# Optimization experiments

Measured on AMD Instinct MI355X. Metric: run time of the kernel, lower is better.

## Reference

```python
import jax, jax.numpy as jnp
import numpy as np

V, E, U, L = 32000, 512, 1024, 2  # vocab, embed_dim, units, layers
B, T = 64, 256


def setup_inputs() -> dict:
    key = jax.random.key(0)
    ks = jax.random.split(key, 8)
    s = lambda k, shape: jax.random.normal(k, shape, jnp.float32) * 0.02
    return {
        "tokens": jax.random.randint(ks[0], (B, T), 0, V),
        "emb": s(ks[1], (V, E)),
        "W0": s(ks[2], (E, 4 * U)), "U0": s(ks[3], (U, 4 * U)),
        "b0": jnp.zeros((4 * U,), jnp.float32),
        "W1": s(ks[4], (U, 4 * U)), "U1": s(ks[5], (U, 4 * U)),
        "b1": jnp.zeros((4 * U,), jnp.float32),
    }


def _lstm_layer(x, W, Uw, b):
    # x: [B,T,D]. Precompute all input projections: [T,B,4U] (batched GEMM outside scan).
    xz = jnp.einsum('btd,dg->tbg', x, W) + b
    units = Uw.shape[0]

    def step(carry, xz_t):
        h, c = carry
        z = xz_t + h @ Uw  # [B,4U]
        i, f, g, o = jnp.split(z, 4, axis=-1)  # Keras gate order: i,f,c,o
        i = jax.nn.sigmoid(i)
        f = jax.nn.sigmoid(f)
        g = jnp.tanh(g)
        o = jax.nn.sigmoid(o)
        c = f * c + i * g
        h = o * jnp.tanh(c)
        return (h, c), h

    h0 = jnp.zeros((x.shape[0], units), x.dtype)
    (h, c), ys = jax.lax.scan(step, (h0, h0), xz)
    return jnp.transpose(ys, (1, 0, 2)), h, c  # [B,T,U], [B,U], [B,U]


def reference(tokens, emb, W0, U0, b0, W1, U1, b1):
    x = emb[tokens]  # [B,T,E] embedding lookup
    x, h, c = _lstm_layer(x, W0, U0, b0)
    x, h, c = _lstm_layer(x, W1, U1, b1)
    # Keras: return_sequences=True, return_state=True -> (seq, h_last, c_last) of last layer
    return (x, h, c)
```

## Files before the change

### kernel.cpp

```cpp
#include <hip/hip_runtime.h>


typedef _Float16 f16;
typedef _Float16 f16x8 __attribute__((ext_vector_type(8)));
typedef _Float16 f16x4 __attribute__((ext_vector_type(4)));
typedef float f32x4 __attribute__((ext_vector_type(4)));

__device__ __forceinline__ f32x4 mfma16x32(f16x8 a, f16x8 b, f32x4 c) {
  return __builtin_amdgcn_mfma_f32_16x16x32_f16(a, b, c, 0, 0, 0);
}

__device__ __forceinline__ void gl_lds16(const void* g, void* l) {
  __builtin_amdgcn_global_load_lds(
      (const __attribute__((address_space(1))) void*)g,
      (__attribute__((address_space(3))) void*)l, 16, 0, 0);
}

__device__ __forceinline__ float sigmoidf_(float x) {
  return 1.0f / (1.0f + expf(-x));
}

__device__ __forceinline__ void st_f16_sc(f16* p, float v) {
  f16 h = (f16)v;
  unsigned u = (unsigned)__builtin_bit_cast(unsigned short, h);
  asm volatile("global_store_short %0, %1, off sc0 sc1"
               :: "v"(p), "v"(u) : "memory");
}
__device__ __forceinline__ void st_b128_sc(f16* p, f16x8 v) {
  asm volatile("global_store_dwordx4 %0, %1, off sc0 sc1"
               :: "v"(p), "v"(v) : "memory");
}

__device__ __forceinline__ unsigned ld_flag(const unsigned* p) {
  return __hip_atomic_load(p, __ATOMIC_RELAXED, __HIP_MEMORY_SCOPE_AGENT);
}
__device__ __forceinline__ void st_flag(unsigned* p, unsigned v) {
  __hip_atomic_store(p, v, __ATOMIC_RELAXED, __HIP_MEMORY_SCOPE_AGENT);
}

__global__ __launch_bounds__(256) void k_transpose_f16(
    const float* __restrict__ S, f16* __restrict__ D, int K, int N) {
  __shared__ float tile[64][65];
  int nk = K >> 6;
  int k0 = (blockIdx.x % nk) << 6;
  int n0 = (blockIdx.x / nk) << 6;
  int tc = threadIdx.x & 63;
  int tq = threadIdx.x >> 6;
#pragma unroll
  for (int r = 0; r < 16; ++r) {
    int kk = tq * 16 + r;
    tile[kk][tc] = S[(size_t)(k0 + kk) * N + (n0 + tc)];
  }
  __syncthreads();
#pragma unroll
  for (int r = 0; r < 16; ++r) {
    int nn = tq * 16 + r;
    D[(size_t)(n0 + nn) * K + (k0 + tc)] = (f16)tile[tc][nn];
  }
}

__global__ __launch_bounds__(256) void k_embed_f16(
    const int* __restrict__ tok, const float* __restrict__ emb,
    f16* __restrict__ A0) {
  int i = blockIdx.x * 256 + threadIdx.x;
  int m = i >> 7;
  int e = (i & 127) << 2;
  int t = m >> 6, b = m & 63;
  int tk = tok[b * 256 + t];
  const float4 v = *(const float4*)(emb + (size_t)tk * 512 + e);
  f16x4 o = {(f16)v.x, (f16)v.y, (f16)v.z, (f16)v.w};
  *(f16x4*)(A0 + (size_t)m * 512 + e) = o;
}

__global__ __launch_bounds__(256) void k_gemm_f16(
    const f16* __restrict__ A, const f16* __restrict__ Bt,
    const float* __restrict__ bias, f16* __restrict__ C,
    int M, int N, int K) {
  __shared__ f16 sA[2][128 * 32];
  __shared__ f16 sB[2][128 * 32];
  const int tid = threadIdx.x, lane = tid & 63, w = tid >> 6;
  const int mb = M >> 7;
  const int bm = blockIdx.x % mb, bn = blockIdx.x / mb;
  const int am0 = bm << 7, bn0 = bn << 7;
  const int wm = w >> 1, wn = w & 1;
  const int srow = lane >> 2, sch = lane & 3;

  f32x4 acc[4][4] = {};
  const int NT = K >> 5;
  int cur = 0;

  auto stage = [&](int kt, int buf) {
#pragma unroll
    for (int q2 = 0; q2 < 2; ++q2) {
      int q = w * 2 + q2;
      int row = q * 16 + srow;
      const f16* ga = A + (size_t)(am0 + row) * K + kt * 32 + sch * 8;
      const f16* gb = Bt + (size_t)(bn0 + row) * K + kt * 32 + sch * 8;
      gl_lds16(ga, (char*)&sA[buf][0] + q * 1024);
      gl_lds16(gb, (char*)&sB[buf][0] + q * 1024);
    }
  };

  stage(0, 0);
  __syncthreads();
  for (int kt = 0; kt < NT; ++kt) {
    if (kt + 1 < NT) stage(kt + 1, cur ^ 1);
    const f16* pa = &sA[cur][(wm * 64 + (lane & 15)) * 32 + (lane >> 4) * 8];
    const f16* pb = &sB[cur][(wn * 64 + (lane & 15)) * 32 + (lane >> 4) * 8];
    f16x8 av[4], bv[4];
#pragma unroll
    for (int mf = 0; mf < 4; ++mf) av[mf] = *(const f16x8*)(pa + mf * 512);
#pragma unroll
    for (int nf = 0; nf < 4; ++nf) bv[nf] = *(const f16x8*)(pb + nf * 512);
#pragma unroll
    for (int mf = 0; mf < 4; ++mf)
#pragma unroll
      for (int nf = 0; nf < 4; ++nf)
        acc[mf][nf] = mfma16x32(av[mf], bv[nf], acc[mf][nf]);
    __syncthreads();
    cur ^= 1;
  }

#pragma unroll
  for (int mf = 0; mf < 4; ++mf)
#pragma unroll
    for (int nf = 0; nf < 4; ++nf) {
      int col = bn0 + wn * 64 + nf * 16 + (lane & 15);
      float bs = bias[col];
#pragma unroll
      for (int r = 0; r < 4; ++r) {
        int row = am0 + wm * 64 + mf * 16 + (lane >> 4) * 4 + r;
        C[(size_t)row * N + col] = (f16)(acc[mf][nf][r] + bs);
      }
    }
}

__global__ __launch_bounds__(256, 2) void k_scan8(
    const f16* __restrict__ XZ, const f16* __restrict__ U0t,
    const f16* __restrict__ W1t, const f16* __restrict__ U1t,
    const float* __restrict__ b1, f16* __restrict__ A1,
    f16* __restrict__ H1h, float* __restrict__ out, unsigned* arr) {
  __shared__ float zred[4224];
  __shared__ __align__(16) f16 hstage[16][16];
  const int tid = threadIdx.x, lane = tid & 63, w = tid >> 6;
  const int j = lane & 15, kg = lane >> 4;
  const int l = (int)blockIdx.x >> 8;
  const int rb = (int)blockIdx.x & 255;
  const int q = rb >> 6, i = rb & 63;
  const int cc = ((i & 7) << 3) + (i >> 3);
  const int u0 = cc * 16, row0 = q * 16;
  const int wko = w * 256 + kg * 8;
  const int aoff = (row0 + j) * 1024 + wko;
  const int erl = tid >> 4, eunit = tid & 15;
  const int erow = row0 + erl, eu = u0 + eunit;
  unsigned* gArr = arr + (size_t)((l * 4 + q) * 64) * 32;
  unsigned* l0Arr = arr + (size_t)(q * 64) * 32;

  f16x8 bv[4][8];
  {
    const f16* RW = l ? U1t : U0t;
#pragma unroll
    for (int n = 0; n < 4; ++n) {
      const f16* bp = RW + (size_t)(n * 1024 + u0 + j) * 1024 + wko;
#pragma unroll
      for (int kt = 0; kt < 8; ++kt)
        bv[n][kt] = *(const f16x8*)(bp + kt * 32);
    }
  }
  float c = 0.0f;

  if (l == 0) {
    float xz[4];
#pragma unroll
    for (int g = 0; g < 4; ++g)
      xz[g] = (float)XZ[(size_t)erow * 4096 + g * 1024 + eu];

    for (int s = 0; s < 256; ++s) {
      f32x4 acc[4] = {};
      if (s > 0) {
        const f16* ap = A1 + (size_t)(s - 1) * 65536 + aoff;
#pragma unroll
        for (int kt = 0; kt < 8; ++kt) {
          f16x8 av = *(const f16x8*)(ap + kt * 32);
#pragma unroll
          for (int n = 0; n < 4; ++n)
            acc[n] = mfma16x32(av, bv[n][kt], acc[n]);
        }
      }
#pragma unroll
      for (int n = 0; n < 4; ++n)
#pragma unroll
        for (int r = 0; r < 4; ++r)
          zred[w * 1056 + (kg * 4 + r) * 66 + n * 16 + j] = acc[n][r];
      __syncthreads();
      float z[4];
#pragma unroll
      for (int g = 0; g < 4; ++g) {
        float sm = xz[g];
#pragma unroll
        for (int wv = 0; wv < 4; ++wv)
          sm += zred[wv * 1056 + erl * 66 + g * 16 + eunit];
        z[g] = sm;
      }
      float gi = sigmoidf_(z[0]), gf = sigmoidf_(z[1]);
      float gg = tanhf(z[2]), go = sigmoidf_(z[3]);
      c = gf * c + gi * gg;
      hstage[erl][eunit] = (f16)(go * tanhf(c));
      __syncthreads();
      if (tid < 32)
        st_b128_sc(&A1[(size_t)(s * 64 + row0 + (tid >> 1)) * 1024 + u0 +
                       (tid & 1) * 8],
                   *(const f16x8*)&hstage[tid >> 1][(tid & 1) * 8]);
      asm volatile("s_waitcnt vmcnt(0)" ::: "memory");
      __syncthreads();

      const unsigned v = (unsigned)s + 1u;
      if (tid == 0) st_flag(&gArr[(unsigned)i * 32u], v);
      float xzn[4] = {0.f, 0.f, 0.f, 0.f};
      if (s + 1 < 256) {
        const f16* xrow = XZ + (size_t)((s + 1) * 64 + erow) * 4096;
#pragma unroll
        for (int g = 0; g < 4; ++g) xzn[g] = (float)xrow[g * 1024 + eu];
      }
      if (tid < 64) {
        while (ld_flag(&gArr[(unsigned)tid * 32u]) < v)
          __builtin_amdgcn_s_sleep(1);
      }
      __syncthreads();
#pragma unroll
      for (int g = 0; g < 4; ++g) xz[g] = xzn[g];
    }
  } else {
    float bias1[4];
#pragma unroll
    for (int g = 0; g < 4; ++g) bias1[g] = b1[g * 1024 + eu];
    const f16* w1p[4];
#pragma unroll
    for (int n = 0; n < 4; ++n)
      w1p[n] = W1t + (size_t)(n * 1024 + u0 + j) * 1024 + wko;

    if (tid < 64) {
      while (ld_flag(&l0Arr[(unsigned)tid * 32u]) < 1u)
        __builtin_amdgcn_s_sleep(1);
    }
    __syncthreads();
    f32x4 accW[4] = {};
    {
      const f16* ap = A1 + aoff;
#pragma unroll
      for (int kt = 0; kt < 8; ++kt) {
        f16x8 av = *(const f16x8*)(ap + kt * 32);
#pragma unroll
        for (int n = 0; n < 4; ++n)
          accW[n] = mfma16x32(av, *(const f16x8*)(w1p[n] + kt * 32),
                              accW[n]);
      }
    }

    for (int t = 0; t < 256; ++t) {
      f32x4 acc[4] = {accW[0], accW[1], accW[2], accW[3]};
      if (t > 0) {
        const f16* hp = H1h + (size_t)(t - 1) * 65536 + aoff;
#pragma unroll
        for (int kt = 0; kt < 8; ++kt) {
          f16x8 av = *(const f16x8*)(hp + kt * 32);
#pragma unroll
          for (int n = 0; n < 4; ++n)
            acc[n] = mfma16x32(av, bv[n][kt], acc[n]);
        }
      }
#pragma unroll
      for (int n = 0; n < 4; ++n)
#pragma unroll
        for (int r = 0; r < 4; ++r)
          zred[w * 1056 + (kg * 4 + r) * 66 + n * 16 + j] = acc[n][r];
      __syncthreads();
      float z[4];
#pragma unroll
      for (int g = 0; g < 4; ++g) {
        float sm = bias1[g];
#pragma unroll
        for (int wv = 0; wv < 4; ++wv)
          sm += zred[wv * 1056 + erl * 66 + g * 16 + eunit];
        z[g] = sm;
      }
      float gi = sigmoidf_(z[0]), gf = sigmoidf_(z[1]);
      float gg = tanhf(z[2]), go = sigmoidf_(z[3]);
      c = gf * c + gi * gg;
      float hn = go * tanhf(c);
      if (t == 255) {
        out[(size_t)erow * 262144 + (size_t)t * 1024 + eu] = hn;
        out[16777216 + erow * 1024 + eu] = hn;
        out[16777216 + 65536 + erow * 1024 + eu] = c;
        break;
      }
      hstage[erl][eunit] = (f16)hn;
      __syncthreads();
      if (tid < 32)
        st_b128_sc(&H1h[(size_t)t * 65536 + (row0 + (tid >> 1)) * 1024 + u0 +
                        (tid & 1) * 8],
                   *(const f16x8*)&hstage[tid >> 1][(tid & 1) * 8]);
      asm volatile("s_waitcnt vmcnt(0)" ::: "memory");
      __syncthreads();

      const unsigned v = (unsigned)t + 1u;
      if (tid == 0) st_flag(&gArr[(unsigned)i * 32u], v);
      out[(size_t)erow * 262144 + (size_t)t * 1024 + eu] = hn;
      if (tid < 64) {
        while (ld_flag(&gArr[(unsigned)tid * 32u]) < v)
          __builtin_amdgcn_s_sleep(1);
      } else if (tid < 128) {
        while (ld_flag(&l0Arr[(unsigned)(tid - 64) * 32u]) < v + 1u)
          __builtin_amdgcn_s_sleep(1);
      }
      __syncthreads();
      {
        const f16* ap = A1 + (size_t)(t + 1) * 65536 + aoff;
        f32x4 tw[4] = {};
#pragma unroll
        for (int kt = 0; kt < 8; ++kt) {
          f16x8 av = *(const f16x8*)(ap + kt * 32);
#pragma unroll
          for (int n = 0; n < 4; ++n)
            tw[n] = mfma16x32(av, *(const f16x8*)(w1p[n] + kt * 32), tw[n]);
        }
#pragma unroll
        for (int n = 0; n < 4; ++n) accW[n] = tw[n];
      }
    }
  }
}

__device__ __forceinline__ void reduce4(const f32x4 acc[4], float* zred,
                                        float z[4]) {
  const int tid = threadIdx.x, lane = tid & 63, w = tid >> 6;
  const int j = lane & 15, kg = lane >> 4;
#pragma unroll
  for (int mf = 0; mf < 4; ++mf)
#pragma unroll
    for (int r = 0; r < 4; ++r)
      zred[w * 1088 + (mf * 16 + kg * 4 + r) * 17 + j] = acc[mf][r];
  __syncthreads();
  const int erow = tid >> 2, euu = tid & 3;
#pragma unroll
  for (int g = 0; g < 4; ++g) {
#pragma unroll
    for (int wv = 0; wv < 4; ++wv)
      z[g] += zred[wv * 1088 + erow * 17 + g * 4 + euu];
  }
}

__device__ __forceinline__ void step_once(
    int s, int u0, const f16x8 bvU0[8], const f16x8 bvW1[8],
    const f16x8 bvU1[8], const float bias1[4], const float xz[4],
    f16* __restrict__ A1, f16* __restrict__ H1h, int hmask,
    float& c0, float& c1, float* __restrict__ out, float* zred) {
  const int tid = threadIdx.x, lane = tid & 63, w = tid >> 6;
  const int j = lane & 15, kg = lane >> 4;
  const int aoff = j * 1024 + w * 256 + kg * 8;
  const int erow = tid >> 2;
  const int eu = u0 + (tid & 3);

  f32x4 accA[4] = {};
  f32x4 accB[4] = {};

  if (s >= 1) {
    const f16* ap = A1 + (size_t)(s - 1) * 65536 + aoff;
#pragma unroll
    for (int kt = 0; kt < 8; ++kt)
#pragma unroll
      for (int mf = 0; mf < 4; ++mf) {
        f16x8 av = *(const f16x8*)(ap + mf * 16384 + kt * 32);
        if (s < 256) accA[mf] = mfma16x32(av, bvU0[kt], accA[mf]);
        accB[mf] = mfma16x32(av, bvW1[kt], accB[mf]);
      }
    if (s >= 2) {
      const f16* hp = H1h + (size_t)((s - 2) & hmask) * 65536 + aoff;
#pragma unroll
      for (int kt = 0; kt < 8; ++kt)
#pragma unroll
        for (int mf = 0; mf < 4; ++mf)
          accB[mf] = mfma16x32(*(const f16x8*)(hp + mf * 16384 + kt * 32),
                               bvU1[kt], accB[mf]);
    }
  }

  if (s < 256) {
    float z[4] = {xz[0], xz[1], xz[2], xz[3]};
    reduce4(accA, zred, z);
    float gi = sigmoidf_(z[0]), gf = sigmoidf_(z[1]);
    float gg = tanhf(z[2]), go = sigmoidf_(z[3]);
    c0 = gf * c0 + gi * gg;
    st_f16_sc(&A1[(size_t)(s * 64 + erow) * 1024 + eu], go * tanhf(c0));
  }
  __syncthreads();

  if (s >= 1) {
    const int t = s - 1;
    float z[4] = {bias1[0], bias1[1], bias1[2], bias1[3]};
    reduce4(accB, zred, z);
    float gi = sigmoidf_(z[0]), gf = sigmoidf_(z[1]);
    float gg = tanhf(z[2]), go = sigmoidf_(z[3]);
    c1 = gf * c1 + gi * gg;
    float hn = go * tanhf(c1);
    st_f16_sc(&H1h[(size_t)(t & hmask) * 65536 + erow * 1024 + eu], hn);
    out[(size_t)erow * 262144 + (size_t)t * 1024 + eu] = hn;
    if (t == 255) {
      out[16777216 + erow * 1024 + eu] = hn;
      out[16777216 + 65536 + erow * 1024 + eu] = c1;
    }
  }
}

__global__ __launch_bounds__(256, 1) void k_step(
    const f16* __restrict__ XZ, const f16* __restrict__ U0t,
    const f16* __restrict__ W1t, const f16* __restrict__ U1t,
    const float* __restrict__ b1, f16* __restrict__ A1,
    f16* __restrict__ H1h, float* __restrict__ C0, float* __restrict__ C1,
    float* __restrict__ out, int s) {
  __shared__ float zred[4352];
  const int tid_ = threadIdx.x, lane_ = tid_ & 63, w_ = tid_ >> 6;
  const int bid_ = (int)blockIdx.x;
  const int i_ = ((bid_ & 7) << 5) + (bid_ >> 3);
  const int u0 = i_ * 4;
  const int j_ = lane_ & 15;
  const int kg_ = lane_ >> 4;
  const int ncol_ = (j_ >> 2) * 1024 + u0 + (j_ & 3);
  const int woff_ = ncol_ * 1024 + w_ * 256 + kg_ * 8;
  f16x8 bvU0[8], bvW1[8], bvU1[8];
#pragma unroll
  for (int kt = 0; kt < 8; ++kt) {
    bvU0[kt] = *(const f16x8*)(U0t + woff_ + kt * 32);
    bvW1[kt] = *(const f16x8*)(W1t + woff_ + kt * 32);
    bvU1[kt] = *(const f16x8*)(U1t + woff_ + kt * 32);
  }
  const int erow_ = tid_ >> 2;
  const int eu_ = u0 + (tid_ & 3);
  float bias1[4];
#pragma unroll
  for (int g = 0; g < 4; ++g) bias1[g] = b1[g * 1024 + eu_];

  float xz[4] = {0.f, 0.f, 0.f, 0.f};
  if (s < 256) {
    const f16* xrow = XZ + (size_t)(s * 64 + erow_) * 4096;
#pragma unroll
    for (int g = 0; g < 4; ++g) xz[g] = (float)xrow[g * 1024 + eu_];
  }
  float c0 = C0[erow_ * 1024 + eu_];
  float c1 = C1[erow_ * 1024 + eu_];
  step_once(s, u0, bvU0, bvW1, bvU1, bias1, xz, A1, H1h, 1, c0, c1, out,
            zred);
  C0[erow_ * 1024 + eu_] = c0;
  C1[erow_ * 1024 + eu_] = c1;
}

extern "C" void kernel_launch(void* const* d_in, const int* in_sizes, int n_in,
                              void* d_out, int out_size, void* d_ws, size_t ws_size,
                              hipStream_t stream) {
  (void)in_sizes; (void)n_in; (void)out_size;
  const int* tokens = (const int*)d_in[0];
  const float* emb = (const float*)d_in[1];
  const float* W0 = (const float*)d_in[2];
  const float* U0 = (const float*)d_in[3];
  const float* b0 = (const float*)d_in[4];
  const float* W1 = (const float*)d_in[5];
  const float* U1 = (const float*)d_in[6];
  const float* b1 = (const float*)d_in[7];
  float* out = (float*)d_out;

  char* p = (char*)d_ws;
  f16* A0 = (f16*)p;   p += (size_t)16384 * 512 * 2;
  f16* A1 = (f16*)p;   p += (size_t)16384 * 1024 * 2;
  f16* W0t = (f16*)p;  p += (size_t)4096 * 512 * 2;
  f16* U0t = (f16*)p;  p += (size_t)4096 * 1024 * 2;
  f16* W1t = (f16*)p;  p += (size_t)4096 * 1024 * 2;
  f16* U1t = (f16*)p;  p += (size_t)4096 * 1024 * 2;
  f16* XZ = (f16*)p;   p += (size_t)16384 * 4096 * 2;
  float* C0 = (float*)p; p += 64 * 1024 * 4;
  float* C1 = (float*)p; p += 64 * 1024 * 4;
  unsigned* arr = (unsigned*)p; p += 8 * 64 * 32 * 4;
  f16* H1h = (f16*)p;
  const size_t need_coop = (size_t)(p - (char*)d_ws) + (size_t)256 * 65536 * 2;

  k_transpose_f16<<<512, 256, 0, stream>>>(W0, W0t, 512, 4096);
  k_transpose_f16<<<1024, 256, 0, stream>>>(U0, U0t, 1024, 4096);
  k_transpose_f16<<<1024, 256, 0, stream>>>(W1, W1t, 1024, 4096);
  k_transpose_f16<<<1024, 256, 0, stream>>>(U1, U1t, 1024, 4096);

  k_embed_f16<<<8192, 256, 0, stream>>>(tokens, emb, A0);

  k_gemm_f16<<<4096, 256, 0, stream>>>(A0, W0t, b0, XZ, 16384, 4096, 512);

  hipMemsetAsync(C0, 0, 64 * 1024 * 4 * 2, stream);
  hipMemsetAsync(arr, 0, 8 * 64 * 32 * 4, stream);

  bool coop_ok = (ws_size >= need_coop);
  if (coop_ok) {
    const f16* XZc = XZ; const f16* U0c = U0t; const f16* W1c = W1t;
    const f16* U1c = U1t; const float* b1c = b1;
    f16* A1p = A1; f16* H1p = H1h; float* outp = out;
    unsigned* ar = arr;
    void* kargs[] = {(void*)&XZc, (void*)&U0c, (void*)&W1c, (void*)&U1c,
                     (void*)&b1c, (void*)&A1p, (void*)&H1p, (void*)&outp,
                     (void*)&ar};
    hipError_t e = hipLaunchCooperativeKernel((const void*)k_scan8, dim3(512),
                                              dim3(256), kargs, 0, stream);
    if (e != hipSuccess) {
      (void)hipGetLastError();
      coop_ok = false;
    }
  }
  if (!coop_ok) {
    for (int s = 0; s <= 256; ++s)
      k_step<<<256, 256, 0, stream>>>(XZ, U0t, W1t, U1t, b1, A1, H1h, C0, C1,
                                      out, s);
  }
}
```

Measured before the change: 2.606 ms.

## Replace all-to-all flag polling with leader-based gather/broadcast barrier per row group

Per-step inter-block synchronization changes from every block polling all 64 peer flags to a two-level scheme. Block i==0 of each group gathers the 64 arrival flags and then writes per-block release flags plus a mirror flag array for layer 1. Other blocks poll a single release flag with one thread, which cuts global-memory polling traffic but adds an extra hop of latency through the leader. Polls are also bounded by an iteration guard, which avoids hangs but could silently break synchronization if it times out.

```diff
diff --git a/kernel.cpp b/kernel.cpp
--- a/kernel.cpp
+++ b/kernel.cpp
@@ -5,6 +5,13 @@
 typedef _Float16 f16x8 __attribute__((ext_vector_type(8)));
 typedef _Float16 f16x4 __attribute__((ext_vector_type(4)));
 typedef float f32x4 __attribute__((ext_vector_type(4)));
+
+#define POLL_GUARD(cond)                                     \
+  {                                                          \
+    unsigned gg_ = 0;                                        \
+    while ((cond) && (++gg_ < (1u << 18)))                   \
+      __builtin_amdgcn_s_sleep(1);                           \
+  }
 
 __device__ __forceinline__ f32x4 mfma16x32(f16x8 a, f16x8 b, f32x4 c) {
   return __builtin_amdgcn_mfma_f32_16x16x32_f16(a, b, c, 0, 0, 0);
@@ -135,11 +142,12 @@
     }
 }
 
-__global__ __launch_bounds__(256, 2) void k_scan8(
+__global__ __launch_bounds__(256, 2) void k_scanB(
     const f16* __restrict__ XZ, const f16* __restrict__ U0t,
     const f16* __restrict__ W1t, const f16* __restrict__ U1t,
     const float* __restrict__ b1, f16* __restrict__ A1,
-    f16* __restrict__ H1h, float* __restrict__ out, unsigned* arr) {
+    f16* __restrict__ H1h, float* __restrict__ out, unsigned* arr,
+    unsigned* mir) {
   __shared__ float zred[4224];
   __shared__ __align__(16) f16 hstage[16][16];
   const int tid = threadIdx.x, lane = tid & 63, w = tid >> 6;
@@ -153,8 +161,8 @@
   const int aoff = (row0 + j) * 1024 + wko;
   const int erl = tid >> 4, eunit = tid & 15;
   const int erow = row0 + erl, eu = u0 + eunit;
-  unsigned* gArr = arr + (size_t)((l * 4 + q) * 64) * 32;
-  unsigned* l0Arr = arr + (size_t)(q * 64) * 32;
+  unsigned* gArr = arr + (size_t)((l * 4 + q) * 128) * 32;
+  unsigned* gMir = mir + (size_t)(q * 64) * 32;
 
   f16x8 bv[4][8];
   {
@@ -222,11 +230,20 @@
 #pragma unroll
         for (int g = 0; g < 4; ++g) xzn[g] = (float)xrow[g * 1024 + eu];
       }
-      if (tid < 64) {
-        while (ld_flag(&gArr[(unsigned)tid * 32u]) < v)
-          __builtin_amdgcn_s_sleep(1);
-      }
-      __syncthreads();
+      if (i == 0) {
+        if (tid >= 1 && tid < 64) {
+          POLL_GUARD(ld_flag(&gArr[(unsigned)tid * 32u]) < v);
+        }
+        __syncthreads();
+        if (tid >= 1 && tid < 64)
+          st_flag(&gArr[((unsigned)tid + 64u) * 32u], v);
+        if (tid < 64) st_flag(&gMir[(unsigned)tid * 32u], v);
+      } else {
+        if (tid == 0) {
+          POLL_GUARD(ld_flag(&gArr[((unsigned)i + 64u) * 32u]) < v);
+        }
+        __syncthreads();
+      }
 #pragma unroll
       for (int g = 0; g < 4; ++g) xz[g] = xzn[g];
     }
@@ -239,9 +256,8 @@
     for (int n = 0; n < 4; ++n)
       w1p[n] = W1t + (size_t)(n * 1024 + u0 + j) * 1024 + wko;
 
-    if (tid < 64) {
-      while (ld_flag(&l0Arr[(unsigned)tid * 32u]) < 1u)
-        __builtin_amdgcn_s_sleep(1);
+    if (tid == 0) {
+      POLL_GUARD(ld_flag(&gMir[(unsigned)i * 32u]) < 1u);
     }
     __syncthreads();
     f32x4 accW[4] = {};
@@ -306,12 +322,21 @@
       const unsigned v = (unsigned)t + 1u;
       if (tid == 0) st_flag(&gArr[(unsigned)i * 32u], v);
       out[(size_t)erow * 262144 + (size_t)t * 1024 + eu] = hn;
-      if (tid < 64) {
-        while (ld_flag(&gArr[(unsigned)tid * 32u]) < v)
-          __builtin_amdgcn_s_sleep(1);
-      } else if (tid < 128) {
-        while (ld_flag(&l0Arr[(unsigned)(tid - 64) * 32u]) < v + 1u)
-          __builtin_amdgcn_s_sleep(1);
+      if (i == 0) {
+        if (tid >= 1 && tid < 64) {
+          POLL_GUARD(ld_flag(&gArr[(unsigned)tid * 32u]) < v);
+        }
+        __syncthreads();
+        if (tid >= 1 && tid < 64)
+          st_flag(&gArr[((unsigned)tid + 64u) * 32u], v);
+      } else {
+        if (tid == 0) {
+          POLL_GUARD(ld_flag(&gArr[((unsigned)i + 64u) * 32u]) < v);
+        }
+        __syncthreads();
+      }
+      if (tid == 0) {
+        POLL_GUARD(ld_flag(&gMir[(unsigned)i * 32u]) < v + 1u);
       }
       __syncthreads();
       {
@@ -478,7 +503,8 @@
   f16* XZ = (f16*)p;   p += (size_t)16384 * 4096 * 2;
   float* C0 = (float*)p; p += 64 * 1024 * 4;
   float* C1 = (float*)p; p += 64 * 1024 * 4;
-  unsigned* arr = (unsigned*)p; p += 8 * 64 * 32 * 4;
+  unsigned* arr = (unsigned*)p; p += 8 * 128 * 32 * 4;
+  unsigned* mir = (unsigned*)p; p += 4 * 64 * 32 * 4;
   f16* H1h = (f16*)p;
   const size_t need_coop = (size_t)(p - (char*)d_ws) + (size_t)256 * 65536 * 2;
 
@@ -492,18 +518,18 @@
   k_gemm_f16<<<4096, 256, 0, stream>>>(A0, W0t, b0, XZ, 16384, 4096, 512);
 
   hipMemsetAsync(C0, 0, 64 * 1024 * 4 * 2, stream);
-  hipMemsetAsync(arr, 0, 8 * 64 * 32 * 4, stream);
+  hipMemsetAsync(arr, 0, (8 * 128 + 4 * 64) * 32 * 4, stream);
 
   bool coop_ok = (ws_size >= need_coop);
   if (coop_ok) {
     const f16* XZc = XZ; const f16* U0c = U0t; const f16* W1c = W1t;
     const f16* U1c = U1t; const float* b1c = b1;
     f16* A1p = A1; f16* H1p = H1h; float* outp = out;
-    unsigned* ar = arr;
+    unsigned* ar = arr; unsigned* mr = mir;
     void* kargs[] = {(void*)&XZc, (void*)&U0c, (void*)&W1c, (void*)&U1c,
                      (void*)&b1c, (void*)&A1p, (void*)&H1p, (void*)&outp,
-                     (void*)&ar};
-    hipError_t e = hipLaunchCooperativeKernel((const void*)k_scan8, dim3(512),
+                     (void*)&ar, (void*)&mr};
+    hipError_t e = hipLaunchCooperativeKernel((const void*)k_scanB, dim3(512),
                                               dim3(256), kargs, 0, stream);
     if (e != hipSuccess) {
       (void)hipGetLastError();
```

Result: slower. 2.659 ms (+2.1%).
